# Performance work log

Measured on AMD Instinct MI355X. Metric: run time of the kernel, lower is better.

## Reference

```python
import jax, jax.numpy as jnp
import numpy as np

B, N, M, H, IN, OUT, NH = 512, 1024, 64, 512, 256, 256, 4
EPS = 1e-8


def setup_inputs() -> dict:
    key = jax.random.key(0)
    ks = jax.random.split(key, 12)
    s = 0.05  # weight scale for numerical stability
    return {
        "in_data": jax.random.normal(ks[0], (B, IN), jnp.float32),
        "memory": jax.random.normal(ks[1], (B, N, M), jnp.float32),
        "prev_reads": jax.random.normal(ks[2], (NH, B, M), jnp.float32),
        "prev_w_r": jnp.zeros((NH, B, N), jnp.float32),
        "prev_w_w": jnp.zeros((NH, B, N), jnp.float32),
        "h0": jnp.zeros((B, H), jnp.float32),
        "c0": jnp.zeros((B, H), jnp.float32),
        "W_ih": jax.random.normal(ks[3], (4 * H, IN + NH * M), jnp.float32) * s,
        "b_ih": jnp.zeros((4 * H,), jnp.float32),
        "W_hh": jax.random.normal(ks[4], (4 * H, H), jnp.float32) * s,
        "b_hh": jnp.zeros((4 * H,), jnp.float32),
        "W_rh": jax.random.normal(ks[5], (NH, M + 6, H), jnp.float32) * s,
        "b_rh": jnp.zeros((NH, M + 6), jnp.float32),
        "W_wh": jax.random.normal(ks[6], (NH, 3 * M + 6, H), jnp.float32) * s,
        "b_wh": jnp.zeros((NH, 3 * M + 6), jnp.float32),
        "W_out": jax.random.normal(ks[7], (OUT, H + NH * M), jnp.float32) * s,
        "b_out": jnp.zeros((OUT,), jnp.float32),
    }


def _address(h, prev_w, mem, W, b):
    # NTM content + location addressing for one head.
    p = h @ W.T + b  # [B, M+6 (+2M for write)]
    k = jnp.tanh(p[:, :M])
    beta = jax.nn.softplus(p[:, M:M + 1])
    g = jax.nn.sigmoid(p[:, M + 1:M + 2])
    sh = jax.nn.softmax(p[:, M + 2:M + 5], axis=-1)  # shifts {-1,0,+1}
    gamma = 1.0 + jax.nn.softplus(p[:, M + 5:M + 6])
    kn = k / (jnp.linalg.norm(k, axis=-1, keepdims=True) + EPS)
    mn = mem / (jnp.linalg.norm(mem, axis=-1, keepdims=True) + EPS)
    wc = jax.nn.softmax(beta * jnp.einsum('bnm,bm->bn', mn, kn), axis=-1)
    wg = g * wc + (1.0 - g) * prev_w
    ws = (sh[:, 0:1] * jnp.roll(wg, 1, axis=-1)
          + sh[:, 1:2] * wg
          + sh[:, 2:3] * jnp.roll(wg, -1, axis=-1))
    wp = ws ** gamma
    w = wp / (jnp.sum(wp, axis=-1, keepdims=True) + EPS)
    return w, p


def reference(in_data, memory, prev_reads, prev_w_r, prev_w_w, h0, c0,
              W_ih, b_ih, W_hh, b_hh, W_rh, b_rh, W_wh, b_wh, W_out, b_out):
    # controller LSTM step on concat(input, prev reads)
    x = jnp.concatenate([in_data, prev_reads.transpose(1, 0, 2).reshape(B, NH * M)], axis=-1)
    gates = x @ W_ih.T + b_ih + h0 @ W_hh.T + b_hh
    i_g, f_g, g_g, o_g = jnp.split(gates, 4, axis=-1)
    c = jax.nn.sigmoid(f_g) * c0 + jax.nn.sigmoid(i_g) * jnp.tanh(g_g)
    h = jax.nn.sigmoid(o_g) * jnp.tanh(c)

    # interleaved read/write heads (read i sees writes of heads < i)
    mem = memory
    reads = []
    for i in range(NH):
        w_r, _ = _address(h, prev_w_r[i], mem, W_rh[i], b_rh[i])
        reads.append(jnp.einsum('bn,bnm->bm', w_r, mem))
        w_w, p = _address(h, prev_w_w[i], mem, W_wh[i], b_wh[i])
        e = jax.nn.sigmoid(p[:, M + 6:2 * M + 6])
        a = jnp.tanh(p[:, 2 * M + 6:3 * M + 6])
        mem = mem * (1.0 - w_w[:, :, None] * e[:, None, :]) + w_w[:, :, None] * a[:, None, :]

    out = jax.nn.sigmoid(
        jnp.concatenate([h] + reads, axis=-1) @ W_out.T + b_out)
    return out
```

## Files before the change

### kernel.cpp

```cpp
#include <hip/hip_runtime.h>
#include <cmath>

#define B_ 512
#define EPS_ 1e-8f

typedef __bf16 bf16x8 __attribute__((ext_vector_type(8)));
typedef float f32x4 __attribute__((ext_vector_type(4)));

__device__ __forceinline__ float sigmoidf_(float x) { return 1.f / (1.f + expf(-x)); }
__device__ __forceinline__ float softplusf_(float x) { return x > 20.f ? x : log1pf(expf(x)); }
__device__ __forceinline__ unsigned f2bf(float x) {
  union { float f; unsigned u; } v; v.f = x;
  unsigned r = v.u + 0x7FFF + ((v.u >> 16) & 1);
  return r >> 16;
}
__device__ __forceinline__ float bfhi2f(unsigned u) { return __uint_as_float(u & 0xffff0000u); }
__device__ __forceinline__ float bflo2f(unsigned u) { return __uint_as_float(u << 16); }

__global__ void k_prep(const float* __restrict__ in_data, const float* __restrict__ prev_reads,
                       const float* __restrict__ h0,
                       const float* __restrict__ W_ih, const float* __restrict__ W_hh,
                       const float* __restrict__ b_ih, const float* __restrict__ b_hh,
                       const float* __restrict__ W_rh, const float* __restrict__ W_wh,
                       const float* __restrict__ W_out,
                       const float* __restrict__ b_rh, const float* __restrict__ b_wh,
                       unsigned short* __restrict__ x2b,
                       unsigned short* __restrict__ Wcatb, float* __restrict__ bcat,
                       unsigned short* __restrict__ W2b, unsigned short* __restrict__ Woutb,
                       float* __restrict__ bcat2) {
  const int stride = gridDim.x * blockDim.x;
  const int t0 = blockIdx.x * blockDim.x + threadIdx.x;
  for (int i = t0; i < 512 * 1024; i += stride) {
    const int b = i >> 10, j = i & 1023;
    float v;
    if (j < 256) v = in_data[(size_t)b * 256 + j];
    else if (j < 512) { const int jj = j - 256; v = prev_reads[(size_t)(jj >> 6) * B_ * 64 + (size_t)b * 64 + (jj & 63)]; }
    else v = h0[(size_t)b * 512 + (j - 512)];
    x2b[i] = (unsigned short)f2bf(v);
  }
  for (int i = t0; i < 2048 * 1024; i += stride) {
    const int j = i >> 10, k = i & 1023;
    Wcatb[i] = (unsigned short)f2bf(k < 512 ? W_ih[(size_t)j * 512 + k] : W_hh[(size_t)j * 512 + (k - 512)]);
  }
  for (int i = t0; i < 2048; i += stride) bcat[i] = b_ih[i] + b_hh[i];
  for (int i = t0; i < 143360; i += stride) W2b[i] = (unsigned short)f2bf(W_rh[i]);
  for (int i = t0; i < 405504; i += stride) W2b[143360 + i] = (unsigned short)f2bf(W_wh[i]);
  for (int i = t0; i < 196608; i += stride) Woutb[i] = (unsigned short)f2bf(W_out[i]);
  for (int i = t0; i < 280; i += stride) bcat2[i] = b_rh[i];
  for (int i = t0; i < 792; i += stride) bcat2[280 + i] = b_wh[i];
}

template <bool SIG>
__global__ __launch_bounds__(64) void k_gemm_mfma(const unsigned short* __restrict__ A, int lda,
                                                  const unsigned short* __restrict__ W,
                                                  const float* __restrict__ bias,
                                                  float* __restrict__ C,
                                                  int Nn, int Kk, int ldc) {
  const int l = threadIdx.x;
  const int m0 = blockIdx.y * 32, n0 = blockIdx.x * 32;
  const int lr = l & 15, lk = (l >> 4) * 8;
  f32x4 acc00 = {0.f, 0.f, 0.f, 0.f}, acc01 = acc00, acc10 = acc00, acc11 = acc00;
  const size_t pa0 = (size_t)(m0 + lr) * lda + lk;
  const size_t pa1 = pa0 + (size_t)16 * lda;
  const bool bok0 = (n0 + lr) < Nn, bok1 = (n0 + 16 + lr) < Nn;
  const size_t pb0 = (size_t)(n0 + lr) * Kk + lk;
  const size_t pb1 = pb0 + (size_t)16 * Kk;
#pragma unroll 4
  for (int k0 = 0; k0 < Kk; k0 += 32) {
    bf16x8 a0 = *(const bf16x8*)(A + pa0 + k0);
    bf16x8 a1 = *(const bf16x8*)(A + pa1 + k0);
    bf16x8 b0 = {}, b1 = {};
    if (bok0) b0 = *(const bf16x8*)(W + pb0 + k0);
    if (bok1) b1 = *(const bf16x8*)(W + pb1 + k0);
    acc00 = __builtin_amdgcn_mfma_f32_16x16x32_bf16(a0, b0, acc00, 0, 0, 0);
    acc01 = __builtin_amdgcn_mfma_f32_16x16x32_bf16(a0, b1, acc01, 0, 0, 0);
    acc10 = __builtin_amdgcn_mfma_f32_16x16x32_bf16(a1, b0, acc10, 0, 0, 0);
    acc11 = __builtin_amdgcn_mfma_f32_16x16x32_bf16(a1, b1, acc11, 0, 0, 0);
  }
  const int orow = (l >> 4) * 4;
  f32x4 accs[2][2] = {{acc00, acc01}, {acc10, acc11}};
#pragma unroll
  for (int mi = 0; mi < 2; ++mi) {
#pragma unroll
    for (int nj = 0; nj < 2; ++nj) {
      const int n = n0 + nj * 16 + lr;
      if (n < Nn) {
        const float bv = bias[n];
#pragma unroll
        for (int r = 0; r < 4; ++r) {
          const int m = m0 + mi * 16 + orow + r;
          float v = accs[mi][nj][r] + bv;
          if (SIG) v = 1.f / (1.f + expf(-v));
          C[(size_t)m * ldc + n] = v;
        }
      }
    }
  }
}

__global__ void k_lstm(const float* __restrict__ gates, const float* __restrict__ c0,
                       unsigned short* __restrict__ Aoutb) {
  const int idx = blockIdx.x * blockDim.x + threadIdx.x;
  const int b = idx >> 9, j = idx & 511;
  const float* g = gates + (size_t)b * 2048;
  const float ig = g[j], fg = g[512 + j], gg = g[1024 + j], og = g[1536 + j];
  const float c = sigmoidf_(fg) * c0[idx] + sigmoidf_(ig) * tanhf(gg);
  Aoutb[(size_t)b * 768 + j] = (unsigned short)f2bf(sigmoidf_(og) * tanhf(c));
}

__global__ __launch_bounds__(1024, 4) void k_mega(const float* __restrict__ mem0,
                                                  const float* __restrict__ P,
                                                  const float* __restrict__ prev_w_r,
                                                  const float* __restrict__ prev_w_w,
                                                  unsigned short* __restrict__ Aoutb) {
  const int b = blockIdx.x;
  const int t = threadIdx.x;
  const int l = t & 63;
  const int w = t >> 6;
  const int lr = l & 15;
  const int rg = l >> 4;
  const int c0 = lr * 4;

  __shared__ unsigned short smem[65536];
  __shared__ float Ar[1024], Aw[1024];
  __shared__ float nrm_s[1024];
  __shared__ float racc[16][64];
  __shared__ float redA[16], redB[16], redC[16];
  __shared__ float knb[8][64];
  __shared__ float parb[8][8];
  __shared__ float eb[4][64], ab[4][64];

  if (w < 8) {
    const int type = w >> 2, head = w & 3;
    const float* p = P + (size_t)b * 1072 + (type == 0 ? head * 70 : 280 + head * 198);
    const float kv = tanhf(p[l]);
    float ss = kv * kv;
#pragma unroll
    for (int off = 32; off > 0; off >>= 1) ss += __shfl_xor(ss, off);
    knb[w][l] = kv / (sqrtf(ss) + EPS_);
    if (l == 0) {
      parb[w][0] = softplusf_(p[64]);
      parb[w][1] = sigmoidf_(p[65]);
      const float s0 = p[66], s1 = p[67], s2 = p[68];
      const float mx = fmaxf(s0, fmaxf(s1, s2));
      const float e0 = expf(s0 - mx), e1 = expf(s1 - mx), e2 = expf(s2 - mx);
      const float inv = 1.f / (e0 + e1 + e2);
      parb[w][2] = e0 * inv; parb[w][3] = e1 * inv; parb[w][4] = e2 * inv;
      parb[w][5] = 1.f + softplusf_(p[69]);
    }
    if (type == 1) {
      eb[head][l] = sigmoidf_(p[70 + l]);
      ab[head][l] = tanhf(p[134 + l]);
    }
  }
  __syncthreads();

  bf16x8 kb0 = {}, kb1 = {};
  {
    const int c = l & 15, ks = (l >> 4) * 8;
    if (c < 8) {
#pragma unroll
      for (int j = 0; j < 8; ++j) {
        kb0[j] = (__bf16)knb[c][ks + j];
        kb1[j] = (__bf16)knb[c][32 + ks + j];
      }
    }
  }

  {
    const float4* src = (const float4*)(mem0 + (size_t)b * 65536);
#pragma unroll 4
    for (int k = 0; k < 16; ++k) {
      const int v = k * 1024 + t;
      const float4 f = src[v];
      const int n = v >> 4, ch = v & 15;
      uint2 pk;
      pk.x = f2bf(f.x) | (f2bf(f.y) << 16);
      pk.y = f2bf(f.z) | (f2bf(f.w) << 16);
      *(uint2*)((char*)smem + n * 128 + (((ch >> 1) ^ (n & 7)) << 4) + ((ch & 1) << 3)) = pk;
    }
  }

  auto score_pass = [&](int hj) {
#pragma unroll
    for (int tt = 0; tt < 4; ++tt) {
      const int tile = w * 4 + tt;
      const int row = tile * 16 + (l & 15);
      const int s0 = l >> 4;
      const bf16x8 a0 = *(const bf16x8*)((char*)smem + row * 128 + ((s0 ^ (row & 7)) << 4));
      const bf16x8 a1 = *(const bf16x8*)((char*)smem + row * 128 + (((s0 + 4) ^ (row & 7)) << 4));
      f32x4 sacc = {0.f, 0.f, 0.f, 0.f}, gacc = {0.f, 0.f, 0.f, 0.f};
      sacc = __builtin_amdgcn_mfma_f32_16x16x32_bf16(a0, kb0, sacc, 0, 0, 0);
      sacc = __builtin_amdgcn_mfma_f32_16x16x32_bf16(a1, kb1, sacc, 0, 0, 0);
      gacc = __builtin_amdgcn_mfma_f32_16x16x32_bf16(a0, a0, gacc, 0, 0, 0);
      gacc = __builtin_amdgcn_mfma_f32_16x16x32_bf16(a1, a1, gacc, 0, 0, 0);
      const int c = l & 15, gq = l >> 4;
      if (c == hj)     *(f32x4*)&Ar[tile * 16 + gq * 4] = sacc;
      if (c == 4 + hj) *(f32x4*)&Aw[tile * 16 + gq * 4] = sacc;
      if ((c >> 2) == gq) nrm_s[tile * 16 + c] = gacc[c & 3];
    }
  };

  __syncthreads();
  score_pass(0);

  const int h = w >> 3;
  const int u = t & 511;
  float* Abuf = h ? Aw : Ar;

  for (int i = 0; i < 4; ++i) {
    __syncthreads();

    const float beta = parb[h * 4 + i][0], g = parb[h * 4 + i][1];
    const float sh0 = parb[h * 4 + i][2], sh1 = parb[h * 4 + i][3], sh2 = parb[h * 4 + i][4];
    const float gamma = parb[h * 4 + i][5];
    const float* prevw = (h ? prev_w_w : prev_w_r) + ((size_t)i * 512 + b) * 1024;

    const float z0 = beta * Abuf[u] / (sqrtf(nrm_s[u]) + EPS_);
    const float z1 = beta * Abuf[u + 512] / (sqrtf(nrm_s[u + 512]) + EPS_);
    float mx = fmaxf(z0, z1);
#pragma unroll
    for (int off = 32; off > 0; off >>= 1) mx = fmaxf(mx, __shfl_xor(mx, off));
    if (l == 0) redA[w] = mx;
    __syncthreads();
    float gmax = redA[h * 8];
#pragma unroll
    for (int j = 1; j < 8; ++j) gmax = fmaxf(gmax, redA[h * 8 + j]);
    const float e0 = __expf(z0 - gmax), e1 = __expf(z1 - gmax);
    float sm = e0 + e1;
#pragma unroll
    for (int off = 32; off > 0; off >>= 1) sm += __shfl_xor(sm, off);
    if (l == 0) redB[w] = sm;
    __syncthreads();
    float gsum = 0.f;
#pragma unroll
    for (int j = 0; j < 8; ++j) gsum += redB[h * 8 + j];
    const float invs = 1.f / gsum;
    const float wg0 = g * (e0 * invs) + (1.f - g) * prevw[u];
    const float wg1 = g * (e1 * invs) + (1.f - g) * prevw[u + 512];
    Abuf[u] = wg0; Abuf[u + 512] = wg1;
    __syncthreads();
    const float ws0 = sh0 * Abuf[(u + 1023) & 1023] + sh1 * wg0 + sh2 * Abuf[(u + 1) & 1023];
    const float ws1 = sh0 * Abuf[(u + 511) & 1023] + sh1 * wg1 + sh2 * Abuf[(u + 513) & 1023];
    float wp0 = (ws0 > 0.f) ? exp2f(gamma * __log2f(ws0)) : 0.f;
    float wp1 = (ws1 > 0.f) ? exp2f(gamma * __log2f(ws1)) : 0.f;
    float sm2 = wp0 + wp1;
#pragma unroll
    for (int off = 32; off > 0; off >>= 1) sm2 += __shfl_xor(sm2, off);
    if (l == 0) redC[w] = sm2;
    __syncthreads();
    float gsum2 = 0.f;
#pragma unroll
    for (int j = 0; j < 8; ++j) gsum2 += redC[h * 8 + j];
    const float inv2 = 1.f / (gsum2 + EPS_);
    Abuf[u] = wp0 * inv2; Abuf[u + 512] = wp1 * inv2;
    __syncthreads();

    float er[4], aa[4];
    if (i < 3) {
      *(f32x4*)er = *(const f32x4*)&eb[i][c0];
      *(f32x4*)aa = *(const f32x4*)&ab[i][c0];
    }
    float rl[4] = {0.f, 0.f, 0.f, 0.f};
#pragma unroll 2
    for (int it = 0; it < 16; ++it) {
      const int n = it * 64 + w * 4 + rg;
      char* p = (char*)smem + n * 128 + (((lr >> 1) ^ (n & 7)) << 4) + ((lr & 1) << 3);
      uint2 pk = *(uint2*)p;
      float v0 = bflo2f(pk.x), v1 = bfhi2f(pk.x);
      float v2 = bflo2f(pk.y), v3 = bfhi2f(pk.y);
      const float wr = Ar[n];
      rl[0] = fmaf(wr, v0, rl[0]); rl[1] = fmaf(wr, v1, rl[1]);
      rl[2] = fmaf(wr, v2, rl[2]); rl[3] = fmaf(wr, v3, rl[3]);
      if (i < 3) {
        const float ww = Aw[n];
        v0 = v0 * (1.f - ww * er[0]) + ww * aa[0];
        v1 = v1 * (1.f - ww * er[1]) + ww * aa[1];
        v2 = v2 * (1.f - ww * er[2]) + ww * aa[2];
        v3 = v3 * (1.f - ww * er[3]) + ww * aa[3];
        pk.x = f2bf(v0) | (f2bf(v1) << 16);
        pk.y = f2bf(v2) | (f2bf(v3) << 16);
        *(uint2*)p = pk;
      }
    }
#pragma unroll
    for (int c = 0; c < 4; ++c) { rl[c] += __shfl_xor(rl[c], 16); rl[c] += __shfl_xor(rl[c], 32); }
    if (rg == 0) *(f32x4*)&racc[w][c0] = *(f32x4*)rl;
    __syncthreads();
    if (i < 3) score_pass(i + 1);
    if (t < 64) {
      float s = 0.f;
#pragma unroll
      for (int wv = 0; wv < 16; ++wv) s += racc[wv][t];
      Aoutb[(size_t)b * 768 + 512 + i * 64 + t] = (unsigned short)f2bf(s);
    }
  }
}

extern "C" void kernel_launch(void* const* d_in, const int* in_sizes, int n_in,
                              void* d_out, int out_size, void* d_ws, size_t ws_size,
                              hipStream_t stream) {
  (void)in_sizes; (void)n_in; (void)out_size; (void)ws_size;
  const float* in_data = (const float*)d_in[0];
  const float* memory = (const float*)d_in[1];
  const float* prev_reads = (const float*)d_in[2];
  const float* prev_w_r = (const float*)d_in[3];
  const float* prev_w_w = (const float*)d_in[4];
  const float* h0 = (const float*)d_in[5];
  const float* c0 = (const float*)d_in[6];
  const float* W_ih = (const float*)d_in[7];
  const float* b_ih = (const float*)d_in[8];
  const float* W_hh = (const float*)d_in[9];
  const float* b_hh = (const float*)d_in[10];
  const float* W_rh = (const float*)d_in[11];
  const float* b_rh = (const float*)d_in[12];
  const float* W_wh = (const float*)d_in[13];
  const float* b_wh = (const float*)d_in[14];
  const float* W_out = (const float*)d_in[15];
  const float* b_out = (const float*)d_in[16];
  float* out = (float*)d_out;

  char* base = (char*)d_ws;
  auto alloc = [&](size_t bytes) -> char* {
    char* p = base; base += (bytes + 255) & ~(size_t)255; return p;
  };
  unsigned short* x2b   = (unsigned short*)alloc((size_t)512 * 1024 * 2);
  unsigned short* Wcatb = (unsigned short*)alloc((size_t)2048 * 1024 * 2);
  float* bcat           = (float*)alloc(2048 * 4);
  float* gates          = (float*)alloc((size_t)512 * 2048 * 4);
  unsigned short* W2b   = (unsigned short*)alloc((size_t)1072 * 512 * 2);
  float* bcat2          = (float*)alloc(1072 * 4);
  unsigned short* Woutb = (unsigned short*)alloc((size_t)256 * 768 * 2);
  float* P              = (float*)alloc((size_t)512 * 1072 * 4);
  unsigned short* Aoutb = (unsigned short*)alloc((size_t)512 * 768 * 2);

  k_prep<<<2048, 256, 0, stream>>>(in_data, prev_reads, h0, W_ih, W_hh, b_ih, b_hh,
                                   W_rh, W_wh, W_out, b_rh, b_wh,
                                   x2b, Wcatb, bcat, W2b, Woutb, bcat2);
  k_gemm_mfma<false><<<dim3(64, 16), 64, 0, stream>>>(x2b, 1024, Wcatb, bcat, gates, 2048, 1024, 2048);
  k_lstm<<<1024, 256, 0, stream>>>(gates, c0, Aoutb);
  k_gemm_mfma<false><<<dim3(34, 16), 64, 0, stream>>>(Aoutb, 768, W2b, bcat2, P, 1072, 512, 1072);
  k_mega<<<512, 1024, 0, stream>>>(memory, P, prev_w_r, prev_w_w, Aoutb);
  k_gemm_mfma<true><<<dim3(8, 16), 64, 0, stream>>>(Aoutb, 768, Woutb, b_out, out, 256, 768, 256);
}
```

Measured before the change: 132.3 us.

## Keep NTM memory tile in registers as MFMA fragments instead of LDS

```diff
diff --git a/kernel.cpp b/kernel.cpp
--- a/kernel.cpp
+++ b/kernel.cpp
@@ -6,6 +6,7 @@
 
 typedef __bf16 bf16x8 __attribute__((ext_vector_type(8)));
 typedef float f32x4 __attribute__((ext_vector_type(4)));
+typedef unsigned uint32x4_ __attribute__((ext_vector_type(4)));
 
 __device__ __forceinline__ float sigmoidf_(float x) { return 1.f / (1.f + expf(-x)); }
 __device__ __forceinline__ float softplusf_(float x) { return x > 20.f ? x : log1pf(expf(x)); }
@@ -16,6 +17,11 @@
 }
 __device__ __forceinline__ float bfhi2f(unsigned u) { return __uint_as_float(u & 0xffff0000u); }
 __device__ __forceinline__ float bflo2f(unsigned u) { return __uint_as_float(u << 16); }
+__device__ __forceinline__ unsigned cvtpk(float a, float b) {
+  unsigned r;
+  asm("v_cvt_pk_bf16_f32 %0, %1, %2" : "=v"(r) : "v"(a), "v"(b));
+  return r;
+}
 
 __global__ void k_prep(const float* __restrict__ in_data, const float* __restrict__ prev_reads,
                        const float* __restrict__ h0,
@@ -108,49 +114,63 @@
   Aoutb[(size_t)b * 768 + j] = (unsigned short)f2bf(sigmoidf_(og) * tanhf(c));
 }
 
-__global__ __launch_bounds__(1024, 4) void k_mega(const float* __restrict__ mem0,
-                                                  const float* __restrict__ P,
-                                                  const float* __restrict__ prev_w_r,
-                                                  const float* __restrict__ prev_w_w,
-                                                  unsigned short* __restrict__ Aoutb) {
+__global__ __launch_bounds__(512, 4) void k_mega(const float* __restrict__ mem0,
+                                                 const float* __restrict__ P,
+                                                 const float* __restrict__ prev_w_r,
+                                                 const float* __restrict__ prev_w_w,
+                                                 unsigned short* __restrict__ Aoutb) {
   const int b = blockIdx.x;
   const int t = threadIdx.x;
   const int l = t & 63;
   const int w = t >> 6;
-  const int lr = l & 15;
-  const int rg = l >> 4;
-  const int c0 = lr * 4;
-
-  __shared__ unsigned short smem[65536];
-  __shared__ float Ar[1024], Aw[1024];
-  __shared__ float nrm_s[1024];
-  __shared__ float racc[16][64];
-  __shared__ float redA[16], redB[16], redC[16];
+  const int p = l & 15;
+  const int q = l >> 4;
+
+  __shared__ float Ar[1024], Aw[1024], nrm_s[1024];
+  __shared__ float racc[8][64];
   __shared__ float knb[8][64];
   __shared__ float parb[8][8];
   __shared__ float eb[4][64], ab[4][64];
-
-  if (w < 8) {
+  __shared__ float redB[8], redC[8];
+
+  uint32x4_ va[8], vb[8];
+  {
+    const float* src = mem0 + (size_t)b * 65536;
+#pragma unroll
+    for (int tt = 0; tt < 8; ++tt) {
+      const float* rp = src + ((w * 8 + tt) * 16 + p) * 64;
+      const float4 f0 = *(const float4*)(rp + q * 8);
+      const float4 f1 = *(const float4*)(rp + q * 8 + 4);
+      const float4 f2 = *(const float4*)(rp + 32 + q * 8);
+      const float4 f3 = *(const float4*)(rp + 32 + q * 8 + 4);
+      va[tt][0] = cvtpk(f0.x, f0.y); va[tt][1] = cvtpk(f0.z, f0.w);
+      va[tt][2] = cvtpk(f1.x, f1.y); va[tt][3] = cvtpk(f1.z, f1.w);
+      vb[tt][0] = cvtpk(f2.x, f2.y); vb[tt][1] = cvtpk(f2.z, f2.w);
+      vb[tt][2] = cvtpk(f3.x, f3.y); vb[tt][3] = cvtpk(f3.z, f3.w);
+    }
+  }
+
+  {
     const int type = w >> 2, head = w & 3;
-    const float* p = P + (size_t)b * 1072 + (type == 0 ? head * 70 : 280 + head * 198);
-    const float kv = tanhf(p[l]);
+    const float* pp = P + (size_t)b * 1072 + (type == 0 ? head * 70 : 280 + head * 198);
+    const float kv = tanhf(pp[l]);
     float ss = kv * kv;
 #pragma unroll
     for (int off = 32; off > 0; off >>= 1) ss += __shfl_xor(ss, off);
     knb[w][l] = kv / (sqrtf(ss) + EPS_);
     if (l == 0) {
-      parb[w][0] = softplusf_(p[64]);
-      parb[w][1] = sigmoidf_(p[65]);
-      const float s0 = p[66], s1 = p[67], s2 = p[68];
+      parb[w][0] = softplusf_(pp[64]);
+      parb[w][1] = sigmoidf_(pp[65]);
+      const float s0 = pp[66], s1 = pp[67], s2 = pp[68];
       const float mx = fmaxf(s0, fmaxf(s1, s2));
       const float e0 = expf(s0 - mx), e1 = expf(s1 - mx), e2 = expf(s2 - mx);
       const float inv = 1.f / (e0 + e1 + e2);
       parb[w][2] = e0 * inv; parb[w][3] = e1 * inv; parb[w][4] = e2 * inv;
-      parb[w][5] = 1.f + softplusf_(p[69]);
+      parb[w][5] = 1.f + softplusf_(pp[69]);
     }
     if (type == 1) {
-      eb[head][l] = sigmoidf_(p[70 + l]);
-      ab[head][l] = tanhf(p[134 + l]);
+      eb[head][l] = sigmoidf_(pp[70 + l]);
+      ab[head][l] = tanhf(pp[134 + l]);
     }
   }
   __syncthreads();
@@ -167,132 +187,166 @@
     }
   }
 
-  {
-    const float4* src = (const float4*)(mem0 + (size_t)b * 65536);
-#pragma unroll 4
-    for (int k = 0; k < 16; ++k) {
-      const int v = k * 1024 + t;
-      const float4 f = src[v];
-      const int n = v >> 4, ch = v & 15;
-      uint2 pk;
-      pk.x = f2bf(f.x) | (f2bf(f.y) << 16);
-      pk.y = f2bf(f.z) | (f2bf(f.w) << 16);
-      *(uint2*)((char*)smem + n * 128 + (((ch >> 1) ^ (n & 7)) << 4) + ((ch & 1) << 3)) = pk;
-    }
-  }
-
   auto score_pass = [&](int hj) {
 #pragma unroll
-    for (int tt = 0; tt < 4; ++tt) {
-      const int tile = w * 4 + tt;
-      const int row = tile * 16 + (l & 15);
-      const int s0 = l >> 4;
-      const bf16x8 a0 = *(const bf16x8*)((char*)smem + row * 128 + ((s0 ^ (row & 7)) << 4));
-      const bf16x8 a1 = *(const bf16x8*)((char*)smem + row * 128 + (((s0 + 4) ^ (row & 7)) << 4));
+    for (int tt = 0; tt < 8; ++tt) {
+      const int tile = w * 8 + tt;
+      const bf16x8 a0 = __builtin_bit_cast(bf16x8, va[tt]);
+      const bf16x8 a1 = __builtin_bit_cast(bf16x8, vb[tt]);
       f32x4 sacc = {0.f, 0.f, 0.f, 0.f}, gacc = {0.f, 0.f, 0.f, 0.f};
       sacc = __builtin_amdgcn_mfma_f32_16x16x32_bf16(a0, kb0, sacc, 0, 0, 0);
       sacc = __builtin_amdgcn_mfma_f32_16x16x32_bf16(a1, kb1, sacc, 0, 0, 0);
       gacc = __builtin_amdgcn_mfma_f32_16x16x32_bf16(a0, a0, gacc, 0, 0, 0);
       gacc = __builtin_amdgcn_mfma_f32_16x16x32_bf16(a1, a1, gacc, 0, 0, 0);
-      const int c = l & 15, gq = l >> 4;
-      if (c == hj)     *(f32x4*)&Ar[tile * 16 + gq * 4] = sacc;
-      if (c == 4 + hj) *(f32x4*)&Aw[tile * 16 + gq * 4] = sacc;
-      if ((c >> 2) == gq) nrm_s[tile * 16 + c] = gacc[c & 3];
+      if (p == hj)        *(f32x4*)&Ar[tile * 16 + q * 4] = sacc;
+      if (p == 4 + hj)    *(f32x4*)&Aw[tile * 16 + q * 4] = sacc;
+      if ((p >> 2) == q)  nrm_s[tile * 16 + p] = gacc[p & 3];
     }
   };
 
+  score_pass(0);
   __syncthreads();
-  score_pass(0);
-
-  const int h = w >> 3;
-  const int u = t & 511;
+
+  const int h = w >> 2;
+  const int th = t & 255;
   float* Abuf = h ? Aw : Ar;
 
   for (int i = 0; i < 4; ++i) {
-    __syncthreads();
-
     const float beta = parb[h * 4 + i][0], g = parb[h * 4 + i][1];
     const float sh0 = parb[h * 4 + i][2], sh1 = parb[h * 4 + i][3], sh2 = parb[h * 4 + i][4];
     const float gamma = parb[h * 4 + i][5];
     const float* prevw = (h ? prev_w_w : prev_w_r) + ((size_t)i * 512 + b) * 1024;
 
-    const float z0 = beta * Abuf[u] / (sqrtf(nrm_s[u]) + EPS_);
-    const float z1 = beta * Abuf[u + 512] / (sqrtf(nrm_s[u + 512]) + EPS_);
-    float mx = fmaxf(z0, z1);
-#pragma unroll
-    for (int off = 32; off > 0; off >>= 1) mx = fmaxf(mx, __shfl_xor(mx, off));
-    if (l == 0) redA[w] = mx;
-    __syncthreads();
-    float gmax = redA[h * 8];
-#pragma unroll
-    for (int j = 1; j < 8; ++j) gmax = fmaxf(gmax, redA[h * 8 + j]);
-    const float e0 = __expf(z0 - gmax), e1 = __expf(z1 - gmax);
-    float sm = e0 + e1;
-#pragma unroll
-    for (int off = 32; off > 0; off >>= 1) sm += __shfl_xor(sm, off);
-    if (l == 0) redB[w] = sm;
-    __syncthreads();
-    float gsum = 0.f;
-#pragma unroll
-    for (int j = 0; j < 8; ++j) gsum += redB[h * 8 + j];
+    float e4[4];
+    float s = 0.f;
+#pragma unroll
+    for (int k = 0; k < 4; ++k) {
+      const int u = th + 256 * k;
+      const float z = beta * Abuf[u] / (sqrtf(nrm_s[u]) + EPS_);
+      e4[k] = __expf(z);
+      s += e4[k];
+    }
+#pragma unroll
+    for (int off = 32; off > 0; off >>= 1) s += __shfl_xor(s, off);
+    if (l == 0) redB[w] = s;
+    __syncthreads();
+    const float gsum = redB[h * 4] + redB[h * 4 + 1] + redB[h * 4 + 2] + redB[h * 4 + 3];
     const float invs = 1.f / gsum;
-    const float wg0 = g * (e0 * invs) + (1.f - g) * prevw[u];
-    const float wg1 = g * (e1 * invs) + (1.f - g) * prevw[u + 512];
-    Abuf[u] = wg0; Abuf[u + 512] = wg1;
-    __syncthreads();
-    const float ws0 = sh0 * Abuf[(u + 1023) & 1023] + sh1 * wg0 + sh2 * Abuf[(u + 1) & 1023];
-    const float ws1 = sh0 * Abuf[(u + 511) & 1023] + sh1 * wg1 + sh2 * Abuf[(u + 513) & 1023];
-    float wp0 = (ws0 > 0.f) ? exp2f(gamma * __log2f(ws0)) : 0.f;
-    float wp1 = (ws1 > 0.f) ? exp2f(gamma * __log2f(ws1)) : 0.f;
-    float sm2 = wp0 + wp1;
-#pragma unroll
-    for (int off = 32; off > 0; off >>= 1) sm2 += __shfl_xor(sm2, off);
-    if (l == 0) redC[w] = sm2;
-    __syncthreads();
-    float gsum2 = 0.f;
-#pragma unroll
-    for (int j = 0; j < 8; ++j) gsum2 += redC[h * 8 + j];
+    float wg4[4];
+#pragma unroll
+    for (int k = 0; k < 4; ++k) {
+      const int u = th + 256 * k;
+      wg4[k] = g * (e4[k] * invs) + (1.f - g) * prevw[u];
+      Abuf[u] = wg4[k];
+    }
+    __syncthreads();
+    float wp4[4];
+    float s2 = 0.f;
+#pragma unroll
+    for (int k = 0; k < 4; ++k) {
+      const int u = th + 256 * k;
+      const float ws = sh0 * Abuf[(u + 1023) & 1023] + sh1 * wg4[k] + sh2 * Abuf[(u + 1) & 1023];
+      wp4[k] = (ws > 0.f) ? exp2f(gamma * __log2f(ws)) : 0.f;
+      s2 += wp4[k];
+    }
+#pragma unroll
+    for (int off = 32; off > 0; off >>= 1) s2 += __shfl_xor(s2, off);
+    if (l == 0) redC[w] = s2;
+    __syncthreads();
+    const float gsum2 = redC[h * 4] + redC[h * 4 + 1] + redC[h * 4 + 2] + redC[h * 4 + 3];
     const float inv2 = 1.f / (gsum2 + EPS_);
-    Abuf[u] = wp0 * inv2; Abuf[u + 512] = wp1 * inv2;
-    __syncthreads();
-
-    float er[4], aa[4];
+#pragma unroll
+    for (int k = 0; k < 4; ++k) Abuf[th + 256 * k] = wp4[k] * inv2;
+    __syncthreads();
+
+    uint32x4_ epk0 = {}, epk1 = {}, apk0 = {}, apk1 = {};
     if (i < 3) {
-      *(f32x4*)er = *(const f32x4*)&eb[i][c0];
-      *(f32x4*)aa = *(const f32x4*)&ab[i][c0];
-    }
-    float rl[4] = {0.f, 0.f, 0.f, 0.f};
-#pragma unroll 2
-    for (int it = 0; it < 16; ++it) {
-      const int n = it * 64 + w * 4 + rg;
-      char* p = (char*)smem + n * 128 + (((lr >> 1) ^ (n & 7)) << 4) + ((lr & 1) << 3);
-      uint2 pk = *(uint2*)p;
-      float v0 = bflo2f(pk.x), v1 = bfhi2f(pk.x);
-      float v2 = bflo2f(pk.y), v3 = bfhi2f(pk.y);
-      const float wr = Ar[n];
-      rl[0] = fmaf(wr, v0, rl[0]); rl[1] = fmaf(wr, v1, rl[1]);
-      rl[2] = fmaf(wr, v2, rl[2]); rl[3] = fmaf(wr, v3, rl[3]);
-      if (i < 3) {
-        const float ww = Aw[n];
-        v0 = v0 * (1.f - ww * er[0]) + ww * aa[0];
-        v1 = v1 * (1.f - ww * er[1]) + ww * aa[1];
-        v2 = v2 * (1.f - ww * er[2]) + ww * aa[2];
-        v3 = v3 * (1.f - ww * er[3]) + ww * aa[3];
-        pk.x = f2bf(v0) | (f2bf(v1) << 16);
-        pk.y = f2bf(v2) | (f2bf(v3) << 16);
-        *(uint2*)p = pk;
+      const f32x4 e0 = *(const f32x4*)&eb[i][q * 8];
+      const f32x4 e1 = *(const f32x4*)&eb[i][q * 8 + 4];
+      const f32x4 e2 = *(const f32x4*)&eb[i][32 + q * 8];
+      const f32x4 e3 = *(const f32x4*)&eb[i][32 + q * 8 + 4];
+      const f32x4 a0_ = *(const f32x4*)&ab[i][q * 8];
+      const f32x4 a1_ = *(const f32x4*)&ab[i][q * 8 + 4];
+      const f32x4 a2_ = *(const f32x4*)&ab[i][32 + q * 8];
+      const f32x4 a3_ = *(const f32x4*)&ab[i][32 + q * 8 + 4];
+      epk0[0] = cvtpk(e0[0], e0[1]); epk0[1] = cvtpk(e0[2], e0[3]);
+      epk0[2] = cvtpk(e1[0], e1[1]); epk0[3] = cvtpk(e1[2], e1[3]);
+      epk1[0] = cvtpk(e2[0], e2[1]); epk1[1] = cvtpk(e2[2], e2[3]);
+      epk1[2] = cvtpk(e3[0], e3[1]); epk1[3] = cvtpk(e3[2], e3[3]);
+      apk0[0] = cvtpk(a0_[0], a0_[1]); apk0[1] = cvtpk(a0_[2], a0_[3]);
+      apk0[2] = cvtpk(a1_[0], a1_[1]); apk0[3] = cvtpk(a1_[2], a1_[3]);
+      apk1[0] = cvtpk(a2_[0], a2_[1]); apk1[1] = cvtpk(a2_[2], a2_[3]);
+      apk1[2] = cvtpk(a3_[0], a3_[1]); apk1[3] = cvtpk(a3_[2], a3_[3]);
+    }
+
+    float r[16] = {0.f, 0.f, 0.f, 0.f, 0.f, 0.f, 0.f, 0.f,
+                   0.f, 0.f, 0.f, 0.f, 0.f, 0.f, 0.f, 0.f};
+#pragma unroll
+    for (int tt = 0; tt < 8; ++tt) {
+      const int row = (w * 8 + tt) * 16 + p;
+      const float wr = Ar[row];
+      const float ww = (i < 3) ? Aw[row] : 0.f;
+#pragma unroll
+      for (int wd = 0; wd < 4; ++wd) {
+        const unsigned uv = va[tt][wd];
+        const float v0 = bflo2f(uv), v1 = bfhi2f(uv);
+        r[wd * 2 + 0] = fmaf(wr, v0, r[wd * 2 + 0]);
+        r[wd * 2 + 1] = fmaf(wr, v1, r[wd * 2 + 1]);
+        if (i < 3) {
+          const unsigned ue = epk0[wd], ua = apk0[wd];
+          const float n0 = fmaf(v0, fmaf(-ww, bflo2f(ue), 1.f), ww * bflo2f(ua));
+          const float n1 = fmaf(v1, fmaf(-ww, bfhi2f(ue), 1.f), ww * bfhi2f(ua));
+          va[tt][wd] = cvtpk(n0, n1);
+        }
       }
-    }
-#pragma unroll
-    for (int c = 0; c < 4; ++c) { rl[c] += __shfl_xor(rl[c], 16); rl[c] += __shfl_xor(rl[c], 32); }
-    if (rg == 0) *(f32x4*)&racc[w][c0] = *(f32x4*)rl;
-    __syncthreads();
+#pragma unroll
+      for (int wd = 0; wd < 4; ++wd) {
+        const unsigned uv = vb[tt][wd];
+        const float v0 = bflo2f(uv), v1 = bfhi2f(uv);
+        r[8 + wd * 2 + 0] = fmaf(wr, v0, r[8 + wd * 2 + 0]);
+        r[8 + wd * 2 + 1] = fmaf(wr, v1, r[8 + wd * 2 + 1]);
+        if (i < 3) {
+          const unsigned ue = epk1[wd], ua = apk1[wd];
+          const float n0 = fmaf(v0, fmaf(-ww, bflo2f(ue), 1.f), ww * bflo2f(ua));
+          const float n1 = fmaf(v1, fmaf(-ww, bfhi2f(ue), 1.f), ww * bfhi2f(ua));
+          vb[tt][wd] = cvtpk(n0, n1);
+        }
+      }
+    }
+
+#pragma unroll
+    for (int j = 0; j < 8; ++j) {
+      const float send = (p & 1) ? r[j] : r[j + 8];
+      r[j] = ((p & 1) ? r[j + 8] : r[j]) + __shfl_xor(send, 1);
+    }
+#pragma unroll
+    for (int j = 0; j < 4; ++j) {
+      const float send = (p & 2) ? r[j] : r[j + 4];
+      r[j] = ((p & 2) ? r[j + 4] : r[j]) + __shfl_xor(send, 2);
+    }
+#pragma unroll
+    for (int j = 0; j < 2; ++j) {
+      const float send = (p & 4) ? r[j] : r[j + 2];
+      r[j] = ((p & 4) ? r[j + 2] : r[j]) + __shfl_xor(send, 4);
+    }
+    {
+      const float send = (p & 8) ? r[0] : r[1];
+      r[0] = ((p & 8) ? r[1] : r[0]) + __shfl_xor(send, 8);
+    }
+    {
+      const int idx = ((p & 1) << 3) | ((p & 2) << 1) | ((p & 4) >> 1) | ((p & 8) >> 3);
+      const int col = (idx & 8) ? (32 + q * 8 + (idx & 7)) : (q * 8 + idx);
+      racc[w][col] = r[0];
+    }
+
     if (i < 3) score_pass(i + 1);
+    __syncthreads();
+
     if (t < 64) {
-      float s = 0.f;
-#pragma unroll
-      for (int wv = 0; wv < 16; ++wv) s += racc[wv][t];
-      Aoutb[(size_t)b * 768 + 512 + i * 64 + t] = (unsigned short)f2bf(s);
+      float s3 = 0.f;
+#pragma unroll
+      for (int wv = 0; wv < 8; ++wv) s3 += racc[wv][t];
+      Aoutb[(size_t)b * 768 + 512 + i * 64 + t] = (unsigned short)f2bf(s3);
     }
   }
 }
@@ -340,6 +394,6 @@
   k_gemm_mfma<false><<<dim3(64, 16), 64, 0, stream>>>(x2b, 1024, Wcatb, bcat, gates, 2048, 1024, 2048);
   k_lstm<<<1024, 256, 0, stream>>>(gates, c0, Aoutb);
   k_gemm_mfma<false><<<dim3(34, 16), 64, 0, stream>>>(Aoutb, 768, W2b, bcat2, P, 1072, 512, 1072);
-  k_mega<<<512, 1024, 0, stream>>>(memory, P, prev_w_r, prev_w_w, Aoutb);
+  k_mega<<<512, 512, 0, stream>>>(memory, P, prev_w_r, prev_w_w, Aoutb);
   k_gemm_mfma<true><<<dim3(8, 16), 64, 0, stream>>>(Aoutb, 768, Woutb, b_out, out, 256, 768, 256);
 }
```

New measurement: 323.5 us. +144.4%, slower.
